# Kernel tuning notes

Measured on AMD Instinct MI355X. Metric: run time of the kernel, lower is better.

## Reference

```python
import jax, jax.numpy as jnp
from jax import lax
import numpy as np

B, W, F, D = 48, 8192, 64, 128  # batch, input_window, c_in, d_model


def setup_inputs() -> dict:
    key = jax.random.key(0)
    k0, k1, k2, k3 = jax.random.split(key, 4)
    x = jax.random.normal(k0, (B, W, F), jnp.float32)
    # ContextConv(c_in->c_in, k=3): conv1d over time, zero 'same' padding (repo layer, assumed standard conv)
    ctx_w = jax.random.normal(k1, (F, F, 3), jnp.float32) * (2.0 / (F * 3)) ** 0.5
    ctx_b = jnp.zeros((F,), jnp.float32)
    # tokenConv: Conv1d(c_in -> d_model, k=3, circular padding, no bias), kaiming fan_in
    token_w = jax.random.normal(k2, (D, F, 3), jnp.float32) * (2.0 / (F * 3)) ** 0.5
    # seW: Linear(c_in -> input_window)
    seW_w = jax.random.normal(k3, (W, F), jnp.float32) * (1.0 / F) ** 0.5
    seW_b = jnp.zeros((W,), jnp.float32)
    return dict(x=x, ctx_w=ctx_w, ctx_b=ctx_b, token_w=token_w, seW_w=seW_w, seW_b=seW_b)


def _conv1d_ncw(x_ncw, w_oiw, padding):
    return lax.conv_general_dilated(
        x_ncw, w_oiw, window_strides=(1,), padding=padding,
        dimension_numbers=("NCW", "OIW", "NCW"))


def reference(x, ctx_w, ctx_b, token_w, seW_w, seW_b):
    # ---- contextConv: (B,W,F) -> (B,W,F), conv over time ----
    xc = _conv1d_ncw(x.transpose(0, 2, 1), ctx_w, [(1, 1)])  # (B,F,W)
    xc = (xc + ctx_b[None, :, None]).transpose(0, 2, 1)       # (B,W,F)

    # ---- structure_embedding (src is detached in torch) ----
    src = lax.stop_gradient(x)
    srcn = src / jnp.linalg.norm(src, axis=-1, keepdims=True)         # row-normalize each timestep
    gram = jnp.einsum('bwf,bwg->bfg', srcn, srcn)                      # batched f x f matmul
    xse = jax.nn.relu(jnp.einsum('bfg,wg->bfw', gram, seW_w) + seW_b[None, None, :])  # (B,F,W)
    xse = xse.transpose(0, 2, 1)                                       # (B,W,F)

    # ---- tokenConv with circular padding ----
    h = (xc + xse).transpose(0, 2, 1)                                  # (B,F,W)
    hp = jnp.pad(h, ((0, 0), (0, 0), (1, 1)), mode='wrap')
    out = _conv1d_ncw(hp, token_w, 'VALID')                            # (B,D,W)
    return out.transpose(0, 2, 1)                                      # (B,W,D)
```

## Files before the change

### kernel.cpp

```cpp
#include <hip/hip_runtime.h>
#include <stdint.h>

#define Bb 48
#define Ww 8192
#define Ff 64
#define Dd 128
#define TWt 64
#define NSLAB 16

#define WS_GRAMP 0u
#define WS_GRAM  12582912u
#define WS_TWT   13369344u
#define WS_CWT   13418496u
#define WS_GBF   13443072u
#define WS_SWB   13836288u
#define WS_XBF   14884864u
#define WS_TOTAL (14884864ull + 50331648ull)

typedef __bf16 bf16x8 __attribute__((ext_vector_type(8)));
typedef float f32x4 __attribute__((ext_vector_type(4)));

__device__ __forceinline__ float bf2f(unsigned short u){
  union { unsigned int i; float f; } v; v.i = ((unsigned int)u) << 16; return v.f;
}
__device__ __forceinline__ unsigned short f2bf(float f){
  union { float f; unsigned int i; } v; v.f = f;
  unsigned int i = v.i;
  return (unsigned short)((i + 0x7fffu + ((i >> 16) & 1u)) >> 16);
}
__device__ __forceinline__ f32x4 mfma16(bf16x8 a, bf16x8 b, f32x4 c){
  return __builtin_amdgcn_mfma_f32_16x16x32_bf16(a, b, c, 0, 0, 0);
}

__global__ __launch_bounds__(256) void pack_weights(const float* __restrict__ ctx_w,
                                                    const float* __restrict__ token_w,
                                                    unsigned short* __restrict__ cwT,
                                                    unsigned short* __restrict__ twT)
{
  int idx = blockIdx.x * 256 + threadIdx.x;
  const int ntw = Dd * 192;
  if (idx < ntw){
    int d = idx / 192, kim = idx % 192;
    int ktap = kim >> 6, fi = kim & 63;
    twT[idx] = f2bf(token_w[(d * Ff + fi) * 3 + ktap]);
  } else if (idx < ntw + Ff * 192){
    int i2 = idx - ntw;
    int f = i2 / 192, kim = i2 % 192;
    int ktap = kim >> 6, fi = kim & 63;
    cwT[i2] = f2bf(ctx_w[(f * Ff + fi) * 3 + ktap]);
  }
}

__global__ __launch_bounds__(256) void convert_sew(const float* __restrict__ src,
                                                   unsigned short* __restrict__ dst)
{
  int i = (blockIdx.x * 256 + threadIdx.x) * 8;
  float4 a0 = *(const float4*)(src + i);
  float4 a1 = *(const float4*)(src + i + 4);
  union { uint4 q; unsigned short s[8]; } u;
  u.s[0]=f2bf(a0.x); u.s[1]=f2bf(a0.y); u.s[2]=f2bf(a0.z); u.s[3]=f2bf(a0.w);
  u.s[4]=f2bf(a1.x); u.s[5]=f2bf(a1.y); u.s[6]=f2bf(a1.z); u.s[7]=f2bf(a1.w);
  *(uint4*)(dst + i) = u.q;
}

__global__ __launch_bounds__(256) void gram_kernel(const float* __restrict__ x,
                                                   float* __restrict__ gramP,
                                                   unsigned short* __restrict__ xbf,
                                                   int writeXbf)
{
  const int b = blockIdx.y;
  const int w_base = blockIdx.x * 512;
  const int t = threadIdx.x;
  const int lane = t & 63;
  const int wave = t >> 6;
  const int lrow = lane & 15;
  const int lk = lane >> 4;

  __shared__ unsigned short st[64 * 72];

  f32x4 acc[4] = {};

  const int wl = t >> 2;
  const int f0 = (t & 3) * 16;

  for (int sc = 0; sc < 8; ++sc) {
    const int w0 = w_base + sc * 64;
    const float* xr = x + ((size_t)b * Ww + (size_t)(w0 + wl)) * Ff + f0;
    float v[16];
    *(float4*)(v)      = *(const float4*)(xr);
    *(float4*)(v + 4)  = *(const float4*)(xr + 4);
    *(float4*)(v + 8)  = *(const float4*)(xr + 8);
    *(float4*)(v + 12) = *(const float4*)(xr + 12);
    if (writeXbf){
      union { uint4 q[2]; unsigned short s[16]; } u;
#pragma unroll
      for (int i = 0; i < 16; ++i) u.s[i] = f2bf(v[i]);
      unsigned short* dst = xbf + ((size_t)b * Ww + (size_t)(w0 + wl)) * Ff + f0;
      *(uint4*)(dst)     = u.q[0];
      *(uint4*)(dst + 8) = u.q[1];
    }
    float ss = 0.f;
#pragma unroll
    for (int i = 0; i < 16; ++i) ss += v[i] * v[i];
    ss += __shfl_xor(ss, 1);
    ss += __shfl_xor(ss, 2);
    float rinv = rsqrtf(ss);
#pragma unroll
    for (int i = 0; i < 16; ++i) st[(f0 + i) * 72 + wl] = f2bf(v[i] * rinv);
    __syncthreads();
#pragma unroll
    for (int kc = 0; kc < 2; ++kc){
      const int kw = kc * 32 + lk * 8;
      bf16x8 bf = *(const bf16x8*)(st + (wave * 16 + lrow) * 72 + kw);
#pragma unroll
      for (int mt = 0; mt < 4; ++mt){
        bf16x8 af = *(const bf16x8*)(st + (mt * 16 + lrow) * 72 + kw);
        acc[mt] = mfma16(af, bf, acc[mt]);
      }
    }
    __syncthreads();
  }

  float* gb = gramP + ((size_t)(blockIdx.x * Bb + b)) * 4096;
#pragma unroll
  for (int mt = 0; mt < 4; ++mt)
#pragma unroll
    for (int r = 0; r < 4; ++r){
      int f = mt * 16 + lk * 4 + r;
      int g = wave * 16 + lrow;
      gb[f * 64 + g] = acc[mt][r];
    }
}

__global__ __launch_bounds__(256) void gram_reduce(const float* __restrict__ gramP,
                                                   float* __restrict__ gram,
                                                   unsigned short* __restrict__ gbf,
                                                   int fast)
{
  int i = blockIdx.x * 256 + threadIdx.x;
  int b = i >> 10;
  int q = i & 1023;
  float sx = 0.f, sy = 0.f, sz = 0.f, sw = 0.f;
#pragma unroll
  for (int sl = 0; sl < NSLAB; ++sl){
    const float4 v = *(const float4*)(gramP + (((size_t)(sl * Bb + b)) << 12) + q * 4);
    sx += v.x; sy += v.y; sz += v.z; sw += v.w;
  }
  float4 s = make_float4(sx, sy, sz, sw);
  *(float4*)(gram + (((size_t)b) << 12) + q * 4) = s;
  if (fast){
    union { unsigned long long u; unsigned short h[4]; } u;
    u.h[0] = f2bf(sx); u.h[1] = f2bf(sy); u.h[2] = f2bf(sz); u.h[3] = f2bf(sw);
    *(unsigned long long*)(gbf + (((size_t)b) << 12) + q * 4) = u.u;
  }
}

#define XSP 72
#define HSP 72
#define OSPF 132

__global__ __launch_bounds__(256) void fused_kernel(
    const float* __restrict__ x,
    const unsigned short* __restrict__ xbf,
    const float* __restrict__ ctx_b,
    const float* __restrict__ seW_w,
    const unsigned short* __restrict__ sWb,
    const float* __restrict__ seW_b,
    const float* __restrict__ gram,
    const unsigned short* __restrict__ gbf,
    const unsigned short* __restrict__ cwT,
    const unsigned short* __restrict__ twT,
    float* __restrict__ out,
    int fast)
{
  const int b = blockIdx.y;
  const int w0 = blockIdx.x * TWt;
  const int t = threadIdx.x;
  const int lane = t & 63;
  const int wave = t >> 6;
  const int lrow = lane & 15;
  const int lk = lane >> 4;

  __shared__ __align__(16) unsigned char smem[16896 + 66 * HSP * 2];
  unsigned short* xs   = (unsigned short*)smem;
  float*          outs = (float*)smem;
  unsigned short* hsh  = (unsigned short*)(smem + 16896);

  if (fast){
    for (int item = t; item < 84 * 8; item += 256){
      int i = item >> 3, seg = item & 7;
      int c = w0 - 2 + i;
      uint4 val = make_uint4(0u,0u,0u,0u);
      if (c >= 0 && c < Ww) val = *(const uint4*)(xbf + ((size_t)b*Ww + c)*Ff + seg*8);
      *(uint4*)(xs + i*XSP + seg*8) = val;
    }
  } else {
    for (int item = t; item < 84 * 8; item += 256){
      int i = item >> 3, seg = item & 7;
      int c = w0 - 2 + i;
      union { uint4 q; unsigned short s[8]; } u;
      if (c >= 0 && c < Ww){
        const float* xr = x + ((size_t)b*Ww + c)*Ff + seg*8;
        float4 a0 = *(const float4*)(xr);
        float4 a1 = *(const float4*)(xr + 4);
        u.s[0]=f2bf(a0.x); u.s[1]=f2bf(a0.y); u.s[2]=f2bf(a0.z); u.s[3]=f2bf(a0.w);
        u.s[4]=f2bf(a1.x); u.s[5]=f2bf(a1.y); u.s[6]=f2bf(a1.z); u.s[7]=f2bf(a1.w);
      } else {
        u.q = make_uint4(0u,0u,0u,0u);
      }
      *(uint4*)(xs + i*XSP + seg*8) = u.q;
    }
  }
  __syncthreads();

  const int nt = wave;
  bf16x8 cw_frag[6];
  {
    const unsigned short* p = cwT + (nt*16 + lrow)*192 + lk*8;
#pragma unroll
    for (int kc = 0; kc < 6; ++kc) cw_frag[kc] = *(const bf16x8*)(p + kc*32);
  }
  bf16x8 se_frag[2];
  if (fast){
    const unsigned short* gp = gbf + (size_t)b*4096 + (nt*16 + lrow)*64;
#pragma unroll
    for (int kc = 0; kc < 2; ++kc) se_frag[kc] = *(const bf16x8*)(gp + kc*32 + lk*8);
  } else {
    const float* gb = gram + (size_t)b * 4096;
#pragma unroll
    for (int kc = 0; kc < 2; ++kc){
      union { bf16x8 v; unsigned short s[8]; } u;
#pragma unroll
      for (int j = 0; j < 8; ++j){
        int g = kc*32 + lk*8 + j;
        u.s[j] = f2bf(gb[g*64 + nt*16 + lrow]);
      }
      se_frag[kc] = u.v;
    }
  }

  f32x4 xc_acc[5] = {};
  f32x4 se_acc[5] = {};

#pragma unroll
  for (int mt = 0; mt < 5; ++mt){
#pragma unroll
    for (int kc = 0; kc < 6; ++kc){
      int kim = kc*32 + lk*8;
      int ktap = kim >> 6, fi = kim & 63;
      bf16x8 a = *(const bf16x8*)(xs + (mt*16 + lrow + ktap)*XSP + fi);
      xc_acc[mt] = mfma16(a, cw_frag[kc], xc_acc[mt]);
    }
    int hc = (w0 - 1 + mt*16 + lrow) & (Ww - 1);
    if (fast){
      const unsigned short* sp = sWb + (size_t)hc * Ff;
#pragma unroll
      for (int kc = 0; kc < 2; ++kc){
        bf16x8 a = *(const bf16x8*)(sp + kc*32 + lk*8);
        se_acc[mt] = mfma16(a, se_frag[kc], se_acc[mt]);
      }
    } else {
      const float* sp = seW_w + (size_t)hc * Ff;
#pragma unroll
      for (int kc = 0; kc < 2; ++kc){
        union { bf16x8 v; unsigned short s[8]; } u;
        float4 a0 = *(const float4*)(sp + kc*32 + lk*8);
        float4 a1 = *(const float4*)(sp + kc*32 + lk*8 + 4);
        u.s[0]=f2bf(a0.x); u.s[1]=f2bf(a0.y); u.s[2]=f2bf(a0.z); u.s[3]=f2bf(a0.w);
        u.s[4]=f2bf(a1.x); u.s[5]=f2bf(a1.y); u.s[6]=f2bf(a1.z); u.s[7]=f2bf(a1.w);
        se_acc[mt] = mfma16(u.v, se_frag[kc], se_acc[mt]);
      }
    }
  }

  {
    float cb = ctx_b[nt*16 + lrow];
#pragma unroll
    for (int mt = 0; mt < 5; ++mt){
#pragma unroll
      for (int r = 0; r < 4; ++r){
        int j = mt*16 + lk*4 + r;
        if (j < 66){
          int hc = (w0 - 1 + j) & (Ww - 1);
          float se = se_acc[mt][r] + seW_b[hc];
          se = se > 0.f ? se : 0.f;
          hsh[j*HSP + nt*16 + lrow] = f2bf(xc_acc[mt][r] + cb + se);
        }
      }
    }
  }
  __syncthreads();

  if (blockIdx.x == 0 || blockIdx.x == (Ww/TWt - 1)){
    const int j  = (blockIdx.x == 0) ? 0 : 65;
    const int hc = (blockIdx.x == 0) ? (Ww - 1) : 0;
    if (t < 64){
      const int f = t;
      float a = ctx_b[f];
      for (int ktap = 0; ktap < 3; ++ktap){
        int c = hc + ktap - 1;
        if (c >= 0 && c < Ww){
          const float* xr = x + ((size_t)b*Ww + c)*Ff;
          const unsigned short* wr = cwT + f*192 + ktap*64;
          for (int fi = 0; fi < 64; ++fi) a += xr[fi] * bf2f(wr[fi]);
        }
      }
      const float* gb = gram + (size_t)b * 4096;
      const float* sp = seW_w + (size_t)hc * Ff;
      float se = seW_b[hc];
      for (int g = 0; g < 64; ++g) se += sp[g] * gb[g*64 + f];
      se = se > 0.f ? se : 0.f;
      hsh[j*HSP + f] = f2bf(a + se);
    }
    __syncthreads();
  }

  bf16x8 tw_frag[2][6];
#pragma unroll
  for (int q = 0; q < 2; ++q){
    const unsigned short* p = twT + ((wave*2 + q)*16 + lrow)*192 + lk*8;
#pragma unroll
    for (int kc = 0; kc < 6; ++kc) tw_frag[q][kc] = *(const bf16x8*)(p + kc*32);
  }
  f32x4 oacc[4][2] = {};
#pragma unroll
  for (int mt = 0; mt < 4; ++mt){
#pragma unroll
    for (int kc = 0; kc < 6; ++kc){
      int kim = kc*32 + lk*8;
      int ktap = kim >> 6, fi = kim & 63;
      bf16x8 a = *(const bf16x8*)(hsh + (mt*16 + lrow + ktap)*HSP + fi);
#pragma unroll
      for (int q = 0; q < 2; ++q)
        oacc[mt][q] = mfma16(a, tw_frag[q][kc], oacc[mt][q]);
    }
  }

#pragma unroll
  for (int h = 0; h < 2; ++h){
    if (h) __syncthreads();
#pragma unroll
    for (int sub = 0; sub < 2; ++sub){
      int mt = h*2 + sub;
#pragma unroll
      for (int q = 0; q < 2; ++q)
#pragma unroll
        for (int r = 0; r < 4; ++r){
          int lw = sub*16 + lk*4 + r;
          int d = (wave*2 + q)*16 + lrow;
          outs[lw*OSPF + d] = oacc[mt][q][r];
        }
    }
    __syncthreads();
    for (int item = t; item < 32 * 32; item += 256){
      int lw = item >> 5, seg = item & 31;
      *(float4*)(out + ((size_t)b*Ww + (size_t)(w0 + h*32 + lw))*Dd + seg*4) =
          *(const float4*)(outs + lw*OSPF + seg*4);
    }
  }
}

extern "C" void kernel_launch(void* const* d_in, const int* in_sizes, int n_in,
                              void* d_out, int out_size, void* d_ws, size_t ws_size,
                              hipStream_t stream)
{
  const float* x       = (const float*)d_in[0];
  const float* ctx_w   = (const float*)d_in[1];
  const float* ctx_b   = (const float*)d_in[2];
  const float* token_w = (const float*)d_in[3];
  const float* seW_w   = (const float*)d_in[4];
  const float* seW_b   = (const float*)d_in[5];
  float* out = (float*)d_out;

  char* ws = (char*)d_ws;
  float*          gramP = (float*)(ws + WS_GRAMP);
  float*          gram  = (float*)(ws + WS_GRAM);
  unsigned short* twT   = (unsigned short*)(ws + WS_TWT);
  unsigned short* cwT   = (unsigned short*)(ws + WS_CWT);
  unsigned short* gbf   = (unsigned short*)(ws + WS_GBF);
  unsigned short* sWb   = (unsigned short*)(ws + WS_SWB);
  unsigned short* xbf   = (unsigned short*)(ws + WS_XBF);

  const int fast = (ws_size >= (size_t)WS_TOTAL) ? 1 : 0;

  pack_weights<<<dim3(144), dim3(256), 0, stream>>>(ctx_w, token_w, cwT, twT);
  if (fast) convert_sew<<<dim3(256), dim3(256), 0, stream>>>(seW_w, sWb);
  gram_kernel<<<dim3(NSLAB, Bb), dim3(256), 0, stream>>>(x, gramP, xbf, fast);
  gram_reduce<<<dim3(192), dim3(256), 0, stream>>>(gramP, gram, gbf, fast);
  fused_kernel<<<dim3(Ww/TWt, Bb), dim3(256), 0, stream>>>(
      x, xbf, ctx_b, seW_w, sWb, seW_b, gram, gbf, cwT, twT, out, fast);
}
```

Baseline: 382.3 us.

## Split x preprocessing into own kernel, stage seW in LDS, write output directly

Adds an xprep kernel that converts x to bf16 and computes per-row inverse norms, so gram_kernel now reads bf16 x plus rinv instead of fp32 x and gets twice as many slabs (NSLAB 32) for more parallelism. The fused kernel stages its seW rows in LDS with coalesced loads, sets a launch bound of four blocks per CU, and writes the output straight from registers, dropping the LDS transpose and its barriers. The trade-offs are an extra pass over x and more partial gram sums to reduce. The direct output stores are scattered 4-byte writes rather than float4 rows, which may cost write efficiency.

```diff
diff --git a/kernel.cpp b/kernel.cpp
--- a/kernel.cpp
+++ b/kernel.cpp
@@ -6,16 +6,17 @@
 #define Ff 64
 #define Dd 128
 #define TWt 64
-#define NSLAB 16
+#define NSLAB 32
 
 #define WS_GRAMP 0u
-#define WS_GRAM  12582912u
-#define WS_TWT   13369344u
-#define WS_CWT   13418496u
-#define WS_GBF   13443072u
-#define WS_SWB   13836288u
-#define WS_XBF   14884864u
-#define WS_TOTAL (14884864ull + 50331648ull)
+#define WS_GRAM  25165824u
+#define WS_TWT   25952256u
+#define WS_CWT   26001408u
+#define WS_GBF   26025984u
+#define WS_SWB   26419200u
+#define WS_RINV  27467776u
+#define WS_XBF   29040640u
+#define WS_TOTAL (29040640ull + 50331648ull)
 
 typedef __bf16 bf16x8 __attribute__((ext_vector_type(8)));
 typedef float f32x4 __attribute__((ext_vector_type(4)));
@@ -63,13 +64,42 @@
   *(uint4*)(dst + i) = u.q;
 }
 
+__global__ __launch_bounds__(256) void xprep(const float* __restrict__ x,
+                                             unsigned short* __restrict__ xbf,
+                                             float* __restrict__ rinvb)
+{
+  int tid = blockIdx.x * 256 + threadIdx.x;
+  int row = tid >> 2;
+  int f0  = (tid & 3) * 16;
+  const float* xr = x + (size_t)row * Ff + f0;
+  float v[16];
+  *(float4*)(v)      = *(const float4*)(xr);
+  *(float4*)(v + 4)  = *(const float4*)(xr + 4);
+  *(float4*)(v + 8)  = *(const float4*)(xr + 8);
+  *(float4*)(v + 12) = *(const float4*)(xr + 12);
+  float ss = 0.f;
+#pragma unroll
+  for (int i = 0; i < 16; ++i) ss += v[i] * v[i];
+  ss += __shfl_xor(ss, 1);
+  ss += __shfl_xor(ss, 2);
+  float rinv = rsqrtf(ss);
+  union { uint4 q[2]; unsigned short s[16]; } u;
+#pragma unroll
+  for (int i = 0; i < 16; ++i) u.s[i] = f2bf(v[i]);
+  unsigned short* dst = xbf + (size_t)row * Ff + f0;
+  *(uint4*)(dst)     = u.q[0];
+  *(uint4*)(dst + 8) = u.q[1];
+  if ((tid & 3) == 0) rinvb[row] = rinv;
+}
+
 __global__ __launch_bounds__(256) void gram_kernel(const float* __restrict__ x,
+                                                   const unsigned short* __restrict__ xbf,
+                                                   const float* __restrict__ rinvb,
                                                    float* __restrict__ gramP,
-                                                   unsigned short* __restrict__ xbf,
-                                                   int writeXbf)
+                                                   int fast)
 {
   const int b = blockIdx.y;
-  const int w_base = blockIdx.x * 512;
+  const int w_base = blockIdx.x * (Ww / NSLAB);
   const int t = threadIdx.x;
   const int lane = t & 63;
   const int wave = t >> 6;
@@ -83,30 +113,34 @@
   const int wl = t >> 2;
   const int f0 = (t & 3) * 16;
 
-  for (int sc = 0; sc < 8; ++sc) {
+  for (int sc = 0; sc < (Ww / NSLAB) / 64; ++sc) {
     const int w0 = w_base + sc * 64;
-    const float* xr = x + ((size_t)b * Ww + (size_t)(w0 + wl)) * Ff + f0;
-    float v[16];
-    *(float4*)(v)      = *(const float4*)(xr);
-    *(float4*)(v + 4)  = *(const float4*)(xr + 4);
-    *(float4*)(v + 8)  = *(const float4*)(xr + 8);
-    *(float4*)(v + 12) = *(const float4*)(xr + 12);
-    if (writeXbf){
-      union { uint4 q[2]; unsigned short s[16]; } u;
-#pragma unroll
-      for (int i = 0; i < 16; ++i) u.s[i] = f2bf(v[i]);
-      unsigned short* dst = xbf + ((size_t)b * Ww + (size_t)(w0 + wl)) * Ff + f0;
-      *(uint4*)(dst)     = u.q[0];
-      *(uint4*)(dst + 8) = u.q[1];
-    }
-    float ss = 0.f;
-#pragma unroll
-    for (int i = 0; i < 16; ++i) ss += v[i] * v[i];
-    ss += __shfl_xor(ss, 1);
-    ss += __shfl_xor(ss, 2);
-    float rinv = rsqrtf(ss);
-#pragma unroll
-    for (int i = 0; i < 16; ++i) st[(f0 + i) * 72 + wl] = f2bf(v[i] * rinv);
+    const size_t rowg = (size_t)b * Ww + (size_t)(w0 + wl);
+    if (fast){
+      union { uint4 q; unsigned short s[8]; } a0, a1;
+      a0.q = *(const uint4*)(xbf + rowg * Ff + f0);
+      a1.q = *(const uint4*)(xbf + rowg * Ff + f0 + 8);
+      float rinv = rinvb[rowg];
+#pragma unroll
+      for (int i = 0; i < 8; ++i) st[(f0 + i) * 72 + wl]     = f2bf(bf2f(a0.s[i]) * rinv);
+#pragma unroll
+      for (int i = 0; i < 8; ++i) st[(f0 + 8 + i) * 72 + wl] = f2bf(bf2f(a1.s[i]) * rinv);
+    } else {
+      const float* xr = x + rowg * Ff + f0;
+      float v[16];
+      *(float4*)(v)      = *(const float4*)(xr);
+      *(float4*)(v + 4)  = *(const float4*)(xr + 4);
+      *(float4*)(v + 8)  = *(const float4*)(xr + 8);
+      *(float4*)(v + 12) = *(const float4*)(xr + 12);
+      float ss = 0.f;
+#pragma unroll
+      for (int i = 0; i < 16; ++i) ss += v[i] * v[i];
+      ss += __shfl_xor(ss, 1);
+      ss += __shfl_xor(ss, 2);
+      float rinv = rsqrtf(ss);
+#pragma unroll
+      for (int i = 0; i < 16; ++i) st[(f0 + i) * 72 + wl] = f2bf(v[i] * rinv);
+    }
     __syncthreads();
 #pragma unroll
     for (int kc = 0; kc < 2; ++kc){
@@ -156,10 +190,10 @@
 }
 
 #define XSP 72
+#define SSP 72
 #define HSP 72
-#define OSPF 132
-
-__global__ __launch_bounds__(256) void fused_kernel(
+
+__global__ __launch_bounds__(256, 4) void fused_kernel(
     const float* __restrict__ x,
     const unsigned short* __restrict__ xbf,
     const float* __restrict__ ctx_b,
@@ -181,10 +215,10 @@
   const int lrow = lane & 15;
   const int lk = lane >> 4;
 
-  __shared__ __align__(16) unsigned char smem[16896 + 66 * HSP * 2];
-  unsigned short* xs   = (unsigned short*)smem;
-  float*          outs = (float*)smem;
-  unsigned short* hsh  = (unsigned short*)(smem + 16896);
+  __shared__ __align__(16) unsigned char smem[(84 * XSP + 80 * SSP + 66 * HSP) * 2];
+  unsigned short* xs  = (unsigned short*)smem;
+  unsigned short* sws = xs + 84 * XSP;
+  unsigned short* hsh = sws + 80 * SSP;
 
   if (fast){
     for (int item = t; item < 84 * 8; item += 256){
@@ -193,6 +227,11 @@
       uint4 val = make_uint4(0u,0u,0u,0u);
       if (c >= 0 && c < Ww) val = *(const uint4*)(xbf + ((size_t)b*Ww + c)*Ff + seg*8);
       *(uint4*)(xs + i*XSP + seg*8) = val;
+    }
+    for (int item = t; item < 80 * 8; item += 256){
+      int i = item >> 3, seg = item & 7;
+      int hc = (w0 - 1 + i) & (Ww - 1);
+      *(uint4*)(sws + i*SSP + seg*8) = *(const uint4*)(sWb + (size_t)hc*Ff + seg*8);
     }
   } else {
     for (int item = t; item < 84 * 8; item += 256){
@@ -251,15 +290,14 @@
       bf16x8 a = *(const bf16x8*)(xs + (mt*16 + lrow + ktap)*XSP + fi);
       xc_acc[mt] = mfma16(a, cw_frag[kc], xc_acc[mt]);
     }
-    int hc = (w0 - 1 + mt*16 + lrow) & (Ww - 1);
     if (fast){
-      const unsigned short* sp = sWb + (size_t)hc * Ff;
 #pragma unroll
       for (int kc = 0; kc < 2; ++kc){
-        bf16x8 a = *(const bf16x8*)(sp + kc*32 + lk*8);
+        bf16x8 a = *(const bf16x8*)(sws + (mt*16 + lrow)*SSP + kc*32 + lk*8);
         se_acc[mt] = mfma16(a, se_frag[kc], se_acc[mt]);
       }
     } else {
+      int hc = (w0 - 1 + mt*16 + lrow) & (Ww - 1);
       const float* sp = seW_w + (size_t)hc * Ff;
 #pragma unroll
       for (int kc = 0; kc < 2; ++kc){
@@ -337,26 +375,15 @@
   }
 
 #pragma unroll
-  for (int h = 0; h < 2; ++h){
-    if (h) __syncthreads();
-#pragma unroll
-    for (int sub = 0; sub < 2; ++sub){
-      int mt = h*2 + sub;
-#pragma unroll
-      for (int q = 0; q < 2; ++q)
-#pragma unroll
-        for (int r = 0; r < 4; ++r){
-          int lw = sub*16 + lk*4 + r;
-          int d = (wave*2 + q)*16 + lrow;
-          outs[lw*OSPF + d] = oacc[mt][q][r];
-        }
-    }
-    __syncthreads();
-    for (int item = t; item < 32 * 32; item += 256){
-      int lw = item >> 5, seg = item & 31;
-      *(float4*)(out + ((size_t)b*Ww + (size_t)(w0 + h*32 + lw))*Dd + seg*4) =
-          *(const float4*)(outs + lw*OSPF + seg*4);
-    }
+  for (int mt = 0; mt < 4; ++mt){
+#pragma unroll
+    for (int q = 0; q < 2; ++q)
+#pragma unroll
+      for (int r = 0; r < 4; ++r){
+        int row = w0 + mt*16 + lk*4 + r;
+        int d   = (wave*2 + q)*16 + lrow;
+        out[((size_t)b*Ww + row)*Dd + d] = oacc[mt][q][r];
+      }
   }
 }
 
@@ -379,13 +406,17 @@
   unsigned short* cwT   = (unsigned short*)(ws + WS_CWT);
   unsigned short* gbf   = (unsigned short*)(ws + WS_GBF);
   unsigned short* sWb   = (unsigned short*)(ws + WS_SWB);
+  float*          rinvb = (float*)(ws + WS_RINV);
   unsigned short* xbf   = (unsigned short*)(ws + WS_XBF);
 
   const int fast = (ws_size >= (size_t)WS_TOTAL) ? 1 : 0;
 
   pack_weights<<<dim3(144), dim3(256), 0, stream>>>(ctx_w, token_w, cwT, twT);
-  if (fast) convert_sew<<<dim3(256), dim3(256), 0, stream>>>(seW_w, sWb);
-  gram_kernel<<<dim3(NSLAB, Bb), dim3(256), 0, stream>>>(x, gramP, xbf, fast);
+  if (fast){
+    convert_sew<<<dim3(256), dim3(256), 0, stream>>>(seW_w, sWb);
+    xprep<<<dim3(6144), dim3(256), 0, stream>>>(x, xbf, rinvb);
+  }
+  gram_kernel<<<dim3(NSLAB, Bb), dim3(256), 0, stream>>>(x, xbf, rinvb, gramP, fast);
   gram_reduce<<<dim3(192), dim3(256), 0, stream>>>(gramP, gram, gbf, fast);
   fused_kernel<<<dim3(Ww/TWt, Bb), dim3(256), 0, stream>>>(
       x, xbf, ctx_b, seW_w, sWb, seW_b, gram, gbf, cwT, twT, out, fast);
```

Measured after the change: 370.8 us. -3.0%, faster.
